# Performance work log

Hardware: AMD Instinct MI355X
Metric: run time of the kernel (lower is better)

## Reference

```python
import jax, jax.numpy as jnp
import numpy as np

B, N, D = 8, 4096, 256
K = 8192

def setup_inputs() -> dict:
    key = jax.random.key(0)
    k1, k2 = jax.random.split(key)
    x = jax.random.normal(k1, (B, N, D), dtype=jnp.float32)
    codebook = jax.random.normal(k2, (K, D), dtype=jnp.float32)
    return {"x": x, "codebook": codebook}

def reference(x, codebook):
    """Euclidean VQ forward: cdist + argmin nearest-codebook assignment,
    straight-through quantization, commitment loss, and the scatter-based
    EMA statistics (cluster counts and per-cluster sums)."""
    b, n, d = x.shape
    k = codebook.shape[0]
    flat = x.reshape(-1, d)                                  # [BN, D]
    x2 = jnp.sum(flat * flat, axis=-1, keepdims=True)        # [BN, 1]
    c2 = jnp.sum(codebook * codebook, axis=-1)               # [K]
    dist = x2 + c2[None, :] - 2.0 * (flat @ codebook.T)      # [BN, K]
    embed_ind = jnp.argmin(dist, axis=-1)                    # [BN]
    quantize = codebook[embed_ind].reshape(b, n, d)          # gather
    # commitment loss (codebook detached, as in EMA codebooks)
    commit_loss = jnp.mean((jax.lax.stop_gradient(quantize) - x) ** 2)
    # straight-through estimator
    quantize_st = x + jax.lax.stop_gradient(quantize - x)
    # EMA codebook-update statistics (scatter / segment reductions)
    cluster_size = jax.ops.segment_sum(
        jnp.ones_like(embed_ind, dtype=x.dtype), embed_ind, num_segments=k)  # [K]
    embed_sum = jax.ops.segment_sum(flat, embed_ind, num_segments=k)         # [K, D]
    return quantize_st, embed_ind.reshape(b, n), commit_loss, cluster_size, embed_sum
```

## Files before the change

### kernel.cpp

```cpp
#include <hip/hip_runtime.h>
#include <hip/hip_bf16.h>
#include <math.h>

#define DIM 256
#define KCODES 8192
#define BN_TOTAL 32768

#define OUT_IND 8388608
#define OUT_LOSS 8421376
#define OUT_CS 8421377
#define OUT_ES 8429569
#define OUT_TOTAL 10526721

#define XI8_OFF 0
#define CI8_OFF 4194304
#define PART_OFF OUT_ES

typedef unsigned short u16;
typedef unsigned char u8;
typedef unsigned int u32;
typedef __attribute__((ext_vector_type(4))) int i32x4;
typedef __attribute__((address_space(1))) const void gvoid_t;
typedef __attribute__((address_space(3))) void lvoid_t;

#define QSCALE (127.0f / 6.0f)
#define INV_2S2 (16129.0f / 72.0f)

__global__ __launch_bounds__(256) void vq_prep(const float* __restrict__ x,
                                               const float* __restrict__ cb,
                                               u8* __restrict__ Xi8,
                                               u8* __restrict__ Ci8,
                                               float* __restrict__ c2,
                                               int* __restrict__ c2i) {
  int b = blockIdx.x;
  bool isx = (b < 2048);
  int g = (isx ? b : (b - 2048)) * 256 + threadIdx.x;
  int row = g >> 4;
  int chunk = g & 15;
  const float* src = (isx ? x : cb) + (size_t)row * DIM + chunk * 16;
  float vv[16];
#pragma unroll
  for (int q = 0; q < 4; ++q) {
    float4 v = *(const float4*)(src + q * 4);
    vv[q * 4 + 0] = v.x; vv[q * 4 + 1] = v.y;
    vv[q * 4 + 2] = v.z; vv[q * 4 + 3] = v.w;
  }
  u32 w[4];
  float s = 0.0f;
#pragma unroll
  for (int q = 0; q < 4; ++q) {
    u32 acc = 0;
#pragma unroll
    for (int e = 0; e < 4; ++e) {
      float v = vv[q * 4 + e];
      s += v * v;
      float vs = fminf(fmaxf(v * QSCALE, -127.0f), 127.0f);
      int iv = (int)rintf(vs);
      acc |= ((u32)(u8)(char)iv) << (8 * e);
    }
    w[q] = acc;
  }
  uint4 pk = {w[0], w[1], w[2], w[3]};
  if (isx) {
    *(uint4*)(Xi8 + (size_t)row * DIM + chunk * 16) = pk;
  } else {
    int kbg = chunk >> 2;
    int j = chunk & 3;
    int js = j ^ ((row >> 1) & 3);
    *(uint4*)(Ci8 + (size_t)row * DIM + kbg * 64 + js * 16) = pk;
#pragma unroll
    for (int m = 1; m <= 8; m <<= 1) s += __shfl_xor(s, m, 64);
    if (chunk == 0) {
      c2[row] = s;
      c2i[row] = (int)rintf((s - 256.0f) * INV_2S2);
    }
  }
}

__global__ __launch_bounds__(256, 4)
void vq_mfma(const u8* __restrict__ XB, const u8* __restrict__ CBb,
             const int* __restrict__ c2i, int2* __restrict__ partials) {
  __shared__ __align__(16) u8 As[2][128][64];
  const int t = threadIdx.x;
  const int wid = t >> 6;
  const int lane = t & 63;
  const int lhi = lane >> 4, llo = lane & 15;
  const int sl = lhi ^ ((llo >> 1) & 3);
  const int wm = wid & 1;
  const int wn = wid >> 1;
  const int rt = blockIdx.x & 511;
  const int s = blockIdx.x >> 9;
  const int row0 = rt * 64;
  const int code0base = s * 4096;

  i32x4 b[2][4];
#pragma unroll
  for (int n = 0; n < 2; ++n) {
    const u8* bp = XB + (size_t)(row0 + wn * 32 + n * 16 + llo) * DIM + lhi * 16;
#pragma unroll
    for (int kb = 0; kb < 4; ++kb)
      b[n][kb] = *(const i32x4*)(bp + kb * 64);
  }

  char* AsB = (char*)As;
  const int srow = lane >> 2;
  const int scol = (lane & 3) << 4;

  int v1[2], v2[2];
#pragma unroll
  for (int n = 0; n < 2; ++n) { v1[n] = 0x7FFFFFFF; v2[n] = 0x7FFFFFFF; }

  auto STAGE = [&](int ct, int kb, int d) {
#pragma unroll
    for (int i = 0; i < 2; ++i) {
      const int p = wid * 2 + i;
      const int cblk = p * 16;
      const u8* sp = CBb + (size_t)(code0base + ct * 128 + cblk + srow) * DIM +
                     kb * 64 + scol;
      char* dp = AsB + (d << 13) + (p << 10);
      __builtin_amdgcn_global_load_lds((gvoid_t*)sp, (lvoid_t*)dp, 16, 0, 0);
    }
  };

  STAGE(0, 0, 0);

#pragma unroll 1
  for (int ct = 0; ct < 32; ++ct) {
    const int code0 = code0base + ct * 128;
    i32x4 acc[4][2];
#pragma unroll
    for (int m = 0; m < 4; ++m)
#pragma unroll
      for (int n = 0; n < 2; ++n) acc[m][n] = (i32x4){0, 0, 0, 0};

#pragma unroll
    for (int kb = 0; kb < 4; ++kb) {
      const int cc = ct * 4 + kb;
      if (cc < 127) {
        const int nct = (kb == 3) ? ct + 1 : ct;
        const int nkb = (kb == 3) ? 0 : kb + 1;
        STAGE(nct, nkb, (cc + 1) & 1);
      }
      __syncthreads();
      const char* src = AsB + ((cc & 1) << 13);
      i32x4 a[4];
#pragma unroll
      for (int m = 0; m < 4; ++m)
        a[m] = *(const i32x4*)(src + ((wm * 64 + m * 16 + llo) << 6) + (sl << 4));
#pragma unroll
      for (int m = 0; m < 4; ++m)
#pragma unroll
        for (int n = 0; n < 2; ++n)
          acc[m][n] = __builtin_amdgcn_mfma_i32_16x16x64_i8(a[m], b[n][kb],
                                                            acc[m][n], 0, 0, 0);
      if (kb == 3) {
#pragma unroll
        for (int m = 0; m < 4; ++m) {
          int cbase = code0 + wm * 64 + m * 16 + lhi * 4;
          int4 cv = *(const int4*)(c2i + cbase);
          int cvv[4] = {cv.x, cv.y, cv.z, cv.w};
#pragma unroll
          for (int n = 0; n < 2; ++n) {
#pragma unroll
            for (int r = 0; r < 4; ++r) {
              int diff = cvv[r] - acc[m][n][r];
              int key = (int)(((u32)diff << 13) + (u32)(cbase + r));
              int ov1 = v1[n];
              v1[n] = min(key, ov1);
              v2[n] = min(v2[n], max(key, ov1));
            }
          }
        }
      }
      __syncthreads();
    }
  }
#pragma unroll
  for (int n = 0; n < 2; ++n) {
    int row = row0 + wn * 32 + n * 16 + llo;
    int slot = s * 8 + wm * 4 + lhi;
    partials[(size_t)row * 16 + slot] = make_int2(v1[n], v2[n]);
  }
}

__global__ __launch_bounds__(256)
void vq_pick(const float* __restrict__ x, const float* __restrict__ cb,
             const float* __restrict__ c2g, const int2* __restrict__ partials,
             int* __restrict__ ind, float* __restrict__ out_ind,
             float* __restrict__ out_q, int* __restrict__ cnt,
             float* __restrict__ loss_part) {
  __shared__ float lsm[4];
  int wid = threadIdx.x >> 6, lane = threadIdx.x & 63;
  int row = blockIdx.x * 4 + wid;
  int cv = 0x7FFFFFFF, cv2 = 0x7FFFFFFF;
  if (lane < 16) {
    int2 p = partials[(size_t)row * 16 + lane];
    cv = p.x; cv2 = p.y;
  }
  int cand[4];
#pragma unroll
  for (int rsel = 0; rsel < 4; ++rsel) {
    int bv = cv;
#pragma unroll
    for (int mask = 1; mask < 16; mask <<= 1)
      bv = min(bv, __shfl_xor(bv, mask, 64));
    bv = __shfl(bv, 0, 64);
    cand[rsel] = bv & 8191;
    if (cv == bv) { cv = cv2; cv2 = 0x7FFFFFFF; }
  }
  const float4 xv = *(const float4*)(x + (size_t)row * DIM + lane * 4);
  float4 q0 = *(const float4*)(cb + (size_t)cand[0] * DIM + lane * 4);
  float4 q1 = *(const float4*)(cb + (size_t)cand[1] * DIM + lane * 4);
  float4 q2 = *(const float4*)(cb + (size_t)cand[2] * DIM + lane * 4);
  float4 q3 = *(const float4*)(cb + (size_t)cand[3] * DIM + lane * 4);
  float d0 = xv.x * q0.x + xv.y * q0.y + xv.z * q0.z + xv.w * q0.w;
  float d1 = xv.x * q1.x + xv.y * q1.y + xv.z * q1.z + xv.w * q1.w;
  float d2 = xv.x * q2.x + xv.y * q2.y + xv.z * q2.z + xv.w * q2.w;
  float d3 = xv.x * q3.x + xv.y * q3.y + xv.z * q3.z + xv.w * q3.w;
  float x2 = xv.x * xv.x + xv.y * xv.y + xv.z * xv.z + xv.w * xv.w;
#pragma unroll
  for (int mask = 1; mask < 64; mask <<= 1) {
    d0 += __shfl_xor(d0, mask, 64);
    d1 += __shfl_xor(d1, mask, 64);
    d2 += __shfl_xor(d2, mask, 64);
    d3 += __shfl_xor(d3, mask, 64);
    x2 += __shfl_xor(x2, mask, 64);
  }
  float e0 = fmaf(-2.0f, d0, c2g[cand[0]]);
  float e1 = fmaf(-2.0f, d1, c2g[cand[1]]);
  float e2 = fmaf(-2.0f, d2, c2g[cand[2]]);
  float e3 = fmaf(-2.0f, d3, c2g[cand[3]]);
  float best = e0; int bk = cand[0];
  if (e1 < best || (e1 == best && cand[1] < bk)) { best = e1; bk = cand[1]; }
  if (e2 < best || (e2 == best && cand[2] < bk)) { best = e2; bk = cand[2]; }
  if (e3 < best || (e3 == best && cand[3] < bk)) { best = e3; bk = cand[3]; }
  float4 q = (bk == cand[1]) ? q1 : (bk == cand[2]) ? q2 : (bk == cand[3]) ? q3 : q0;
  *(float4*)(out_q + (size_t)row * DIM + lane * 4) = q;
  if (lane == 0) {
    ind[row] = bk;
    out_ind[row] = (float)bk;
    atomicAdd(cnt + bk, 1);
    lsm[wid] = x2 + best;
  }
  __syncthreads();
  if (threadIdx.x == 0)
    loss_part[blockIdx.x] = lsm[0] + lsm[1] + lsm[2] + lsm[3];
}

__global__ __launch_bounds__(1024)
void vq_scan(const int* __restrict__ cnt, int* __restrict__ offs,
             int* __restrict__ woffs, float* __restrict__ out_cs,
             const float* __restrict__ loss_part, float* __restrict__ out_loss) {
  __shared__ int ssum[1024];
  __shared__ float sls[1024];
  int tid = threadIdx.x;
  int c[8], loc[8];
  int s = 0;
#pragma unroll
  for (int j = 0; j < 8; ++j) {
    c[j] = cnt[tid * 8 + j];
    loc[j] = s;
    s += c[j];
  }
  ssum[tid] = s;
  float ls = 0.0f;
#pragma unroll
  for (int j = 0; j < 8; ++j) ls += loss_part[tid * 8 + j];
  sls[tid] = ls;
  __syncthreads();
  for (int off = 1; off < 1024; off <<= 1) {
    int v = (tid >= off) ? ssum[tid - off] : 0;
    __syncthreads();
    ssum[tid] += v;
    __syncthreads();
  }
  int base = (tid > 0) ? ssum[tid - 1] : 0;
#pragma unroll
  for (int j = 0; j < 8; ++j) {
    int o = base + loc[j];
    offs[tid * 8 + j] = o;
    woffs[tid * 8 + j] = o;
    out_cs[tid * 8 + j] = (float)c[j];
  }
  for (int off = 512; off >= 1; off >>= 1) {
    if (tid < off) sls[tid] += sls[tid + off];
    __syncthreads();
  }
  if (tid == 0) *out_loss = sls[0] * (1.0f / 8388608.0f);
}

__global__ __launch_bounds__(256)
void vq_scatter(const int* __restrict__ ind, int* __restrict__ woffs,
                int* __restrict__ rowlist) {
  int row = blockIdx.x * 256 + threadIdx.x;
  int k = ind[row];
  int pos = atomicAdd(woffs + k, 1);
  rowlist[pos] = row;
}

__global__ __launch_bounds__(256)
void vq_esum(const float* __restrict__ x, const int* __restrict__ offs,
             const int* __restrict__ cnt, const int* __restrict__ rowlist,
             float* __restrict__ out_es) {
  __shared__ float4 sred[3][64];
  int k = blockIdx.x;
  int wid = threadIdx.x >> 6, lane = threadIdx.x & 63;
  int start = offs[k], n = cnt[k];
  const int* rl = rowlist + start;
  int jb = (n * wid) >> 2, je = (n * (wid + 1)) >> 2;
  float4 acc = {0.f, 0.f, 0.f, 0.f};
  int j = jb;
  for (; j + 4 <= je; j += 4) {
    int r0 = rl[j], r1 = rl[j + 1], r2 = rl[j + 2], r3 = rl[j + 3];
    float4 v0 = *(const float4*)(x + (size_t)r0 * DIM + lane * 4);
    float4 v1 = *(const float4*)(x + (size_t)r1 * DIM + lane * 4);
    float4 v2 = *(const float4*)(x + (size_t)r2 * DIM + lane * 4);
    float4 v3 = *(const float4*)(x + (size_t)r3 * DIM + lane * 4);
    acc.x += v0.x + v1.x + v2.x + v3.x;
    acc.y += v0.y + v1.y + v2.y + v3.y;
    acc.z += v0.z + v1.z + v2.z + v3.z;
    acc.w += v0.w + v1.w + v2.w + v3.w;
  }
  for (; j < je; ++j) {
    int r = rl[j];
    float4 v = *(const float4*)(x + (size_t)r * DIM + lane * 4);
    acc.x += v.x; acc.y += v.y; acc.z += v.z; acc.w += v.w;
  }
  if (wid > 0) sred[wid - 1][lane] = acc;
  __syncthreads();
  if (wid == 0) {
    float4 a1 = sred[0][lane], a2 = sred[1][lane], a3 = sred[2][lane];
    acc.x += a1.x + a2.x + a3.x;
    acc.y += a1.y + a2.y + a3.y;
    acc.z += a1.z + a2.z + a3.z;
    acc.w += a1.w + a2.w + a3.w;
    *(float4*)(out_es + (size_t)k * DIM + lane * 4) = acc;
  }
}

extern "C" void kernel_launch(void* const* d_in, const int* in_sizes, int n_in,
                              void* d_out, int out_size, void* d_ws,
                              size_t ws_size, hipStream_t stream) {
  const float* x = (const float*)d_in[0];
  const float* cb = (const float*)d_in[1];
  float* out = (float*)d_out;
  float* out_q = out;
  float* out_ind = out + OUT_IND;
  float* out_loss = out + OUT_LOSS;
  float* out_cs = out + OUT_CS;
  float* out_es = out + OUT_ES;

  u8* Xi8 = (u8*)(out + XI8_OFF);
  u8* Ci8 = (u8*)(out + CI8_OFF);
  int2* partials = (int2*)(out + PART_OFF);

  char* w = (char*)d_ws;
  int* cnt = (int*)w;
  int* offs = (int*)(w + (32 << 10));
  int* woffs = (int*)(w + (64 << 10));
  float* loss_part = (float*)(w + (96 << 10));
  int* ind = (int*)(w + (128 << 10));
  int* rowlist = (int*)(w + (256 << 10));
  float* c2 = (float*)(w + (384 << 10));
  int* c2i = (int*)(w + (416 << 10));

  hipMemsetAsync(cnt, 0, KCODES * sizeof(int), stream);
  vq_prep<<<2560, 256, 0, stream>>>(x, cb, Xi8, Ci8, c2, c2i);
  vq_mfma<<<1024, 256, 0, stream>>>(Xi8, Ci8, c2i, partials);
  vq_pick<<<BN_TOTAL / 4, 256, 0, stream>>>(x, cb, c2, partials, ind, out_ind,
                                            out_q, cnt, loss_part);
  vq_scan<<<1, 1024, 0, stream>>>(cnt, offs, woffs, out_cs, loss_part, out_loss);
  vq_scatter<<<BN_TOTAL / 256, 256, 0, stream>>>(ind, woffs, rowlist);
  vq_esum<<<KCODES, 256, 0, stream>>>(x, offs, cnt, rowlist, out_es);
}
```

Before: 184.5 us.

## Issue next codebook tile load after barrier and drop second per-step sync

The loop now does one barrier per k-step instead of two. The barrier comes first, and only then does the loop start the async global-to-LDS load of the next tile into the other buffer. That load can now overlap the current MFMA work, instead of being waited on by the barrier right after it was issued. Staging addresses are also precomputed as base pointers plus a running offset, which cuts per-iteration index arithmetic. Correctness relies on the single barrier both waiting on the outstanding loads and ordering the previous reads before the buffer is overwritten.

Measured after the change: 178.0 us. -3.5%, faster.

```diff
diff --git a/kernel.cpp b/kernel.cpp
--- a/kernel.cpp
+++ b/kernel.cpp
@@ -106,23 +106,25 @@
   const int srow = lane >> 2;
   const int scol = (lane & 3) << 4;
 
+  const int p0 = wid * 2, p1 = wid * 2 + 1;
+  const u8* lb0 = CBb + (size_t)(code0base + p0 * 16 + srow) * DIM + scol;
+  const u8* lb1 = CBb + (size_t)(code0base + p1 * 16 + srow) * DIM + scol;
+  char* dp0 = AsB + (p0 << 10);
+  char* dp1 = AsB + (p1 << 10);
+
+  auto STAGE = [&](u32 srcoff, int d) {
+    __builtin_amdgcn_global_load_lds((gvoid_t*)(lb0 + srcoff),
+                                     (lvoid_t*)(dp0 + (d << 13)), 16, 0, 0);
+    __builtin_amdgcn_global_load_lds((gvoid_t*)(lb1 + srcoff),
+                                     (lvoid_t*)(dp1 + (d << 13)), 16, 0, 0);
+  };
+
   int v1[2], v2[2];
 #pragma unroll
   for (int n = 0; n < 2; ++n) { v1[n] = 0x7FFFFFFF; v2[n] = 0x7FFFFFFF; }
 
-  auto STAGE = [&](int ct, int kb, int d) {
-#pragma unroll
-    for (int i = 0; i < 2; ++i) {
-      const int p = wid * 2 + i;
-      const int cblk = p * 16;
-      const u8* sp = CBb + (size_t)(code0base + ct * 128 + cblk + srow) * DIM +
-                     kb * 64 + scol;
-      char* dp = AsB + (d << 13) + (p << 10);
-      __builtin_amdgcn_global_load_lds((gvoid_t*)sp, (lvoid_t*)dp, 16, 0, 0);
-    }
-  };
-
-  STAGE(0, 0, 0);
+  STAGE(0, 0);
+  u32 ctoff = 0;
 
 #pragma unroll 1
   for (int ct = 0; ct < 32; ++ct) {
@@ -136,12 +138,11 @@
 #pragma unroll
     for (int kb = 0; kb < 4; ++kb) {
       const int cc = ct * 4 + kb;
+      __syncthreads();
       if (cc < 127) {
-        const int nct = (kb == 3) ? ct + 1 : ct;
-        const int nkb = (kb == 3) ? 0 : kb + 1;
-        STAGE(nct, nkb, (cc + 1) & 1);
+        u32 noff = (kb == 3) ? (ctoff + 32768u) : (ctoff + (u32)(kb + 1) * 64u);
+        STAGE(noff, (cc + 1) & 1);
       }
-      __syncthreads();
       const char* src = AsB + ((cc & 1) << 13);
       i32x4 a[4];
 #pragma unroll
@@ -172,8 +173,8 @@
           }
         }
       }
-      __syncthreads();
     }
+    ctoff += 32768u;
   }
 #pragma unroll
   for (int n = 0; n < 2; ++n) {
```
